# Performance work log

Measured on AMD Instinct MI355X. Metric: run time of the kernel, lower is better.

The kernel has to match this reference:

```python
import jax, jax.numpy as jnp
import numpy as np

B, E, V, L = 16384, 16, 1_000_000, 50
DENSE, ONEHOT, MULTIHOT = 13, 26, 2
UNITS = [64, 12]
NN_IN = E * (ONEHOT + MULTIHOT) + DENSE  # 16*28+13 = 461
CONCAT_IN = 1 + E + UNITS[-1]            # 29


def setup_inputs() -> dict:
    key = jax.random.key(0)
    ks = jax.random.split(key, 12)
    s = 0.02  # glorot-ish init scale
    return {
        "dense": jax.random.normal(ks[0], (B, DENSE), jnp.float32),
        "onehot": jax.random.randint(ks[1], (B, ONEHOT), 0, V, jnp.int32),
        "multihot_ids": jax.random.randint(ks[2], (B, MULTIHOT, L), 0, V, jnp.int32),
        "multihot_mask": jnp.ones((B, MULTIHOT, L), jnp.float32),
        "fm_w": jax.random.normal(ks[3], (V, 1), jnp.float32) * s,
        "fm_emb": jax.random.normal(ks[4], (V, E), jnp.float32) * s,
        "nn_w0": jax.random.normal(ks[5], (NN_IN, UNITS[0]), jnp.float32) * s,
        "nn_b0": jnp.zeros((UNITS[0],), jnp.float32),
        "nn_w1": jax.random.normal(ks[6], (UNITS[0], UNITS[1]), jnp.float32) * s,
        "nn_b1": jnp.zeros((UNITS[1],), jnp.float32),
        "concat_w": jax.random.normal(ks[7], (CONCAT_IN, 1), jnp.float32) * s,
        "concat_b": jnp.zeros((1,), jnp.float32),
    }


def reference(dense, onehot, multihot_ids, multihot_mask, fm_w, fm_emb,
              nn_w0, nn_b0, nn_w1, nn_b1, concat_w, concat_b):
    # --- embedding lookups ---
    onehot_emb = fm_emb[onehot]                      # [B, 26, E]
    mh_emb = fm_emb[multihot_ids]                    # [B, 2, L, E]
    m = multihot_mask[..., None]                     # [B, 2, L, 1]
    # embedding_lookup_sparse(combiner='mean') over valid slots; empty rows -> 0 (tf.pad)
    denom = jnp.maximum(jnp.sum(m, axis=2), 1.0)     # [B, 2, 1]
    multihot_emb = jnp.sum(mh_emb * m, axis=2) / denom  # [B, 2, E]
    cat_emb = jnp.concatenate([onehot_emb, multihot_emb], axis=1)  # [B, 28, E]

    # --- FM 1st order: sum_i w_i (x_i = 1) ---
    fm_1st = jnp.sum(fm_w[onehot], axis=1)           # [B, 1]

    # --- FM 2nd order (keep_k_dims=True): 0.5*((sum v)^2 - sum v^2) ---
    s = jnp.sum(cat_emb, axis=1)                     # [B, E]
    fm_2nd = 0.5 * (s * s - jnp.sum(cat_emb * cat_emb, axis=1))  # [B, E]

    # --- deep part ---
    nn_inp = jnp.concatenate([cat_emb.reshape(-1, E * (ONEHOT + MULTIHOT)), dense], axis=1)
    h = jax.nn.relu(nn_inp @ nn_w0 + nn_b0)
    h = jax.nn.relu(h @ nn_w1 + nn_b1)               # [B, 12]

    concat_inp = jnp.concatenate([fm_1st, fm_2nd, h], axis=1)  # [B, 29]
    return jax.nn.sigmoid(concat_inp @ concat_w + concat_b)    # [B, 1]
```

## Files before the change

### kernel.cpp

```cpp
#include <hip/hip_runtime.h>
#include <hip/hip_bf16.h>

#define BATCH 16384
#define EDIM  16
#define NOH   26
#define LL    50
#define KIN   461
#define KPAD  480
#define KLDS  488

using bf16x8 = __attribute__((ext_vector_type(8))) short;
using f32x4  = __attribute__((ext_vector_type(4))) float;

static __device__ __forceinline__ unsigned short f2bf(float f) {
    union { float f; unsigned int u; } v; v.f = f;
    unsigned int r = v.u + 0x7FFFu + ((v.u >> 16) & 1u);
    return (unsigned short)(r >> 16);
}

__global__ __launch_bounds__(1024) void fused(
    const float* __restrict__ dense,
    const int*   __restrict__ onehot,
    const int*   __restrict__ mh_ids,
    const float* __restrict__ mh_mask,
    const float* __restrict__ fm_w,
    const float* __restrict__ fm_emb,
    const float* __restrict__ w0,
    const float* __restrict__ b0,
    const float* __restrict__ w1,
    const float* __restrict__ b1,
    const float* __restrict__ concat_w,
    const float* __restrict__ concat_b,
    float* __restrict__ out)
{
    __shared__ unsigned short As[64 * KLDS];
    __shared__ unsigned short w0s[30720];
    __shared__ float h0s[64][68];
    __shared__ float w1t[12 * 64];
    __shared__ float part_s[64];
    __shared__ float b0s[64];
    __shared__ float b1s[12];
    __shared__ float cwh[12];

    const int t  = threadIdx.x;
    const int wv = t >> 6;
    const int l  = t & 63;
    const int s  = l >> 2;
    const int d  = l & 3;
    const int row0 = blockIdx.x << 6;

    for (int idx = t; idx < 30720; idx += 1024) {
        int j    = idx & 7;
        int frag = idx >> 3;
        int lane = frag & 63;
        int tile = frag >> 6;
        int nt = tile / 15;
        int kt = tile - nt * 15;
        int k = kt * 32 + ((lane >> 4) << 3) + j;
        int n = (nt << 4) + (lane & 15);
        float v = (k < KIN) ? w0[k * 64 + n] : 0.f;
        w0s[idx] = f2bf(v);
    }
    if (t < 768) { int k = t / 12, j = t - k * 12; w1t[j * 64 + k] = w1[t]; }
    if (t < 64)  b0s[t] = b0[t];
    if (t >= 64 && t < 76)   b1s[t - 64] = b1[t - 64];
    if (t >= 96 && t < 108)  cwh[t - 96] = concat_w[17 + (t - 96)];

    for (int i = 0; i < 4; ++i) {
        const int r = (wv << 2) + i;
        const int b = row0 + r;

        const float v1 = (s < 10) ? 1.f : 0.f;
        int oid0 = onehot[b * NOH + s];
        int oid1 = (s < 10) ? onehot[b * NOH + 16 + s] : 0;

        int   mid[7]; float mmk[7];
        #pragma unroll
        for (int p = 0; p < 7; ++p) {
            int pi = p * 16 + s;
            bool valid = pi < 100;
            int f = (pi >= 50) ? 1 : 0;
            int ii = pi - f * 50;
            size_t off = ((size_t)b * 2 + f) * LL + ii;
            mid[p] = valid ? mh_ids[off]  : 0;
            mmk[p] = valid ? mh_mask[off] : 0.f;
        }

        float4 e0 = *(const float4*)(fm_emb + (size_t)oid0 * EDIM + d * 4);
        float4 e1 = *(const float4*)(fm_emb + (size_t)oid1 * EDIM + d * 4);
        float  wsa = fm_w[oid0];
        float  wsb = fm_w[oid1];
        float4 gm[7];
        #pragma unroll
        for (int p = 0; p < 7; ++p)
            gm[p] = *(const float4*)(fm_emb + (size_t)mid[p] * EDIM + d * 4);

        e1.x *= v1; e1.y *= v1; e1.z *= v1; e1.w *= v1;
        float wsum = (d == 0) ? (wsa + v1 * wsb) : 0.f;

        unsigned short* rowp = As + r * KLDS;
        {
            ushort4 u; u.x = f2bf(e0.x); u.y = f2bf(e0.y); u.z = f2bf(e0.z); u.w = f2bf(e0.w);
            *(ushort4*)(rowp + s * EDIM + d * 4) = u;
        }
        if (s < 10) {
            ushort4 u; u.x = f2bf(e1.x); u.y = f2bf(e1.y); u.z = f2bf(e1.z); u.w = f2bf(e1.w);
            *(ushort4*)(rowp + (16 + s) * EDIM + d * 4) = u;
        }

        float a0x=0,a0y=0,a0z=0,a0w=0, a1x=0,a1y=0,a1z=0,a1w=0, m0=0, m1=0;
        #pragma unroll
        for (int p = 0; p < 7; ++p) {
            int pi = p * 16 + s;
            float m = mmk[p];
            if (pi >= 50) { a1x += m*gm[p].x; a1y += m*gm[p].y; a1z += m*gm[p].z; a1w += m*gm[p].w; m1 += m; }
            else          { a0x += m*gm[p].x; a0y += m*gm[p].y; a0z += m*gm[p].z; a0w += m*gm[p].w; m0 += m; }
        }

        float ohx = e0.x + e1.x, ohy = e0.y + e1.y, ohz = e0.z + e1.z, ohw = e0.w + e1.w;
        float qx = e0.x*e0.x + e1.x*e1.x, qy = e0.y*e0.y + e1.y*e1.y;
        float qz = e0.z*e0.z + e1.z*e1.z, qw = e0.w*e0.w + e1.w*e1.w;

#define R4(v) { v += __shfl_xor(v, 4); v += __shfl_xor(v, 8); v += __shfl_xor(v, 16); v += __shfl_xor(v, 32); }
        R4(a0x) R4(a0y) R4(a0z) R4(a0w)
        R4(a1x) R4(a1y) R4(a1z) R4(a1w)
        R4(m0)  R4(m1)
        R4(ohx) R4(ohy) R4(ohz) R4(ohw)
        R4(qx)  R4(qy)  R4(qz)  R4(qw)
        R4(wsum)
#undef R4

        float inv0 = 1.f / fmaxf(m0, 1.f);
        float inv1 = 1.f / fmaxf(m1, 1.f);
        float h0x = a0x*inv0, h0y = a0y*inv0, h0z = a0z*inv0, h0w = a0w*inv0;
        float h1x = a1x*inv1, h1y = a1y*inv1, h1z = a1z*inv1, h1w = a1w*inv1;

        if (s == 0) {
            ushort4 u; u.x = f2bf(h0x); u.y = f2bf(h0y); u.z = f2bf(h0z); u.w = f2bf(h0w);
            *(ushort4*)(rowp + 26 * EDIM + d * 4) = u;
        }
        if (s == 1) {
            ushort4 u; u.x = f2bf(h1x); u.y = f2bf(h1y); u.z = f2bf(h1z); u.w = f2bf(h1w);
            *(ushort4*)(rowp + 27 * EDIM + d * 4) = u;
        }

        float sx = ohx + h0x + h1x, sy = ohy + h0y + h1y, sz = ohz + h0z + h1z, sw = ohw + h0w + h1w;
        float tx = qx + h0x*h0x + h1x*h1x, ty = qy + h0y*h0y + h1y*h1y;
        float tz = qz + h0z*h0z + h1z*h1z, tw = qw + h0w*h0w + h1w*h1w;
        float f2x = 0.5f * (sx*sx - tx), f2y = 0.5f * (sy*sy - ty);
        float f2z = 0.5f * (sz*sz - tz), f2w = 0.5f * (sw*sw - tw);

        float cw0 = concat_w[0];
        float c0 = concat_w[1 + d*4 + 0], c1 = concat_w[1 + d*4 + 1];
        float c2 = concat_w[1 + d*4 + 2], c3 = concat_w[1 + d*4 + 3];
        float part = f2x*c0 + f2y*c1 + f2z*c2 + f2w*c3 + wsum * cw0;
        part += __shfl_xor(part, 1);
        part += __shfl_xor(part, 2);
        if (l == 0) part_s[r] = part + concat_b[0];

        if (l < 32) {
            float v = (l < 13) ? dense[b * 13 + l] : 0.f;
            rowp[448 + l] = f2bf(v);
        }
    }
    __syncthreads();

    const int rt = wv >> 2, nt = wv & 3;
    const int c = l & 15, g = l >> 4;

    f32x4 acc = {0.f, 0.f, 0.f, 0.f};
    const unsigned short* ap = As + (rt * 16 + c) * KLDS + (g << 3);
    const bf16x8* bp = (const bf16x8*)w0s + nt * 15 * 64 + l;

    #pragma unroll
    for (int kt = 0; kt < 15; ++kt) {
        bf16x8 a = *(const bf16x8*)(ap + kt * 32);
        acc = __builtin_amdgcn_mfma_f32_16x16x32_bf16(a, bp[kt * 64], acc, 0, 0, 0);
    }

    #pragma unroll
    for (int reg = 0; reg < 4; ++reg)
        h0s[rt * 16 + g * 4 + reg][nt * 16 + c] = fmaxf(acc[reg] + b0s[nt * 16 + c], 0.f);
    __syncthreads();

    if (wv < 4) {
        float s0 = b1s[g*3 + 0], s1 = b1s[g*3 + 1], s2 = b1s[g*3 + 2];
        #pragma unroll
        for (int k4 = 0; k4 < 16; ++k4) {
            float4 h  = *(const float4*)&h0s[wv * 16 + c][k4 * 4];
            float4 wa = *(const float4*)&w1t[(g*3 + 0) * 64 + k4 * 4];
            float4 wb = *(const float4*)&w1t[(g*3 + 1) * 64 + k4 * 4];
            float4 wc = *(const float4*)&w1t[(g*3 + 2) * 64 + k4 * 4];
            s0 += h.x*wa.x + h.y*wa.y + h.z*wa.z + h.w*wa.w;
            s1 += h.x*wb.x + h.y*wb.y + h.z*wb.z + h.w*wb.w;
            s2 += h.x*wc.x + h.y*wc.y + h.z*wc.z + h.w*wc.w;
        }
        float hd = fmaxf(s0, 0.f)*cwh[g*3] + fmaxf(s1, 0.f)*cwh[g*3+1] + fmaxf(s2, 0.f)*cwh[g*3+2];
        hd += __shfl_xor(hd, 16);
        hd += __shfl_xor(hd, 32);
        if (g == 0) {
            int rr = row0 + wv * 16 + c;
            float x = part_s[wv * 16 + c] + hd;
            out[rr] = 1.f / (1.f + __expf(-x));
        }
    }
}

extern "C" void kernel_launch(void* const* d_in, const int* in_sizes, int n_in,
                              void* d_out, int out_size, void* d_ws, size_t ws_size,
                              hipStream_t stream) {
    const float* dense   = (const float*)d_in[0];
    const int*   onehot  = (const int*)  d_in[1];
    const int*   mh_ids  = (const int*)  d_in[2];
    const float* mh_mask = (const float*)d_in[3];
    const float* fm_w    = (const float*)d_in[4];
    const float* fm_emb  = (const float*)d_in[5];
    const float* w0      = (const float*)d_in[6];
    const float* b0      = (const float*)d_in[7];
    const float* w1      = (const float*)d_in[8];
    const float* b1      = (const float*)d_in[9];
    const float* cw      = (const float*)d_in[10];
    const float* cb      = (const float*)d_in[11];

    hipLaunchKernelGGL(fused, dim3(BATCH / 64), dim3(1024), 0, stream,
                       dense, onehot, mh_ids, mh_mask, fm_w, fm_emb,
                       w0, b0, w1, b1, cw, cb, (float*)d_out);
}
```

Baseline: 165.0 us.

## Pre-swizzle W0 to bf16 in a prep kernel and shrink blocks to 32 rows

A small prep kernel converts and swizzles W0 into MFMA fragment order in workspace once per call, so each block no longer rebuilds a 60KB LDS copy. The fused kernel now handles 32 rows per block with 512 threads, reads W0 fragments straight from global memory (L2-resident), and stores the hidden layer as bf16. The goal is to cut per-block LDS footprint and setup work so more blocks can stay resident and the gather latency is hidden better. In exchange it adds an extra launch, more global or L2 traffic for W0, and some extra rounding of the hidden activations.

```diff
diff --git a/kernel.cpp b/kernel.cpp
--- a/kernel.cpp
+++ b/kernel.cpp
@@ -8,6 +8,7 @@
 #define KIN   461
 #define KPAD  480
 #define KLDS  488
+#define ROWS  32
 
 using bf16x8 = __attribute__((ext_vector_type(8))) short;
 using f32x4  = __attribute__((ext_vector_type(4))) float;
@@ -17,39 +18,15 @@
     unsigned int r = v.u + 0x7FFFu + ((v.u >> 16) & 1u);
     return (unsigned short)(r >> 16);
 }
-
-__global__ __launch_bounds__(1024) void fused(
-    const float* __restrict__ dense,
-    const int*   __restrict__ onehot,
-    const int*   __restrict__ mh_ids,
-    const float* __restrict__ mh_mask,
-    const float* __restrict__ fm_w,
-    const float* __restrict__ fm_emb,
-    const float* __restrict__ w0,
-    const float* __restrict__ b0,
-    const float* __restrict__ w1,
-    const float* __restrict__ b1,
-    const float* __restrict__ concat_w,
-    const float* __restrict__ concat_b,
-    float* __restrict__ out)
-{
-    __shared__ unsigned short As[64 * KLDS];
-    __shared__ unsigned short w0s[30720];
-    __shared__ float h0s[64][68];
-    __shared__ float w1t[12 * 64];
-    __shared__ float part_s[64];
-    __shared__ float b0s[64];
-    __shared__ float b1s[12];
-    __shared__ float cwh[12];
-
-    const int t  = threadIdx.x;
-    const int wv = t >> 6;
-    const int l  = t & 63;
-    const int s  = l >> 2;
-    const int d  = l & 3;
-    const int row0 = blockIdx.x << 6;
-
-    for (int idx = t; idx < 30720; idx += 1024) {
+static __device__ __forceinline__ float bf2f(unsigned short u) {
+    union { unsigned int u; float f; } v; v.u = ((unsigned int)u) << 16;
+    return v.f;
+}
+
+__global__ __launch_bounds__(256) void prep(const float* __restrict__ w0,
+                                            unsigned short* __restrict__ w0f) {
+    int idx = blockIdx.x * 256 + threadIdx.x;
+    if (idx < 30720) {
         int j    = idx & 7;
         int frag = idx >> 3;
         int lane = frag & 63;
@@ -59,12 +36,44 @@
         int k = kt * 32 + ((lane >> 4) << 3) + j;
         int n = (nt << 4) + (lane & 15);
         float v = (k < KIN) ? w0[k * 64 + n] : 0.f;
-        w0s[idx] = f2bf(v);
-    }
-    if (t < 768) { int k = t / 12, j = t - k * 12; w1t[j * 64 + k] = w1[t]; }
-    if (t < 64)  b0s[t] = b0[t];
-    if (t >= 64 && t < 76)   b1s[t - 64] = b1[t - 64];
-    if (t >= 96 && t < 108)  cwh[t - 96] = concat_w[17 + (t - 96)];
+        w0f[idx] = f2bf(v);
+    }
+}
+
+__global__ __launch_bounds__(512, 4) void fused(
+    const float* __restrict__ dense,
+    const int*   __restrict__ onehot,
+    const int*   __restrict__ mh_ids,
+    const float* __restrict__ mh_mask,
+    const float* __restrict__ fm_w,
+    const float* __restrict__ fm_emb,
+    const unsigned short* __restrict__ w0f,
+    const float* __restrict__ b0,
+    const float* __restrict__ w1,
+    const float* __restrict__ b1,
+    const float* __restrict__ concat_w,
+    const float* __restrict__ concat_b,
+    float* __restrict__ out)
+{
+    __shared__ unsigned short As[ROWS * KLDS];
+    __shared__ unsigned short h0s[ROWS][68];
+    __shared__ float w1t[12 * 64];
+    __shared__ float part_s[ROWS];
+    __shared__ float b0s[64];
+    __shared__ float b1s[12];
+    __shared__ float cwh[12];
+
+    const int t  = threadIdx.x;
+    const int wv = t >> 6;
+    const int l  = t & 63;
+    const int s  = l >> 2;
+    const int d  = l & 3;
+    const int row0 = blockIdx.x << 5;
+
+    for (int i = t; i < 768; i += 512) { int k = i / 12, j = i - k * 12; w1t[j * 64 + k] = w1[i]; }
+    if (t < 64)               b0s[t] = b0[t];
+    if (t >= 64 && t < 76)    b1s[t - 64] = b1[t - 64];
+    if (t >= 96 && t < 108)   cwh[t - 96] = concat_w[17 + (t - 96)];
 
     for (int i = 0; i < 4; ++i) {
         const int r = (wv << 2) + i;
@@ -170,30 +179,36 @@
 
     f32x4 acc = {0.f, 0.f, 0.f, 0.f};
     const unsigned short* ap = As + (rt * 16 + c) * KLDS + (g << 3);
-    const bf16x8* bp = (const bf16x8*)w0s + nt * 15 * 64 + l;
+    const unsigned short* bgp = w0f + ((size_t)(nt * 15) * 64 + l) * 8;
 
     #pragma unroll
     for (int kt = 0; kt < 15; ++kt) {
         bf16x8 a = *(const bf16x8*)(ap + kt * 32);
-        acc = __builtin_amdgcn_mfma_f32_16x16x32_bf16(a, bp[kt * 64], acc, 0, 0, 0);
+        bf16x8 bb = *(const bf16x8*)(bgp + (size_t)kt * 64 * 8);
+        acc = __builtin_amdgcn_mfma_f32_16x16x32_bf16(a, bb, acc, 0, 0, 0);
     }
 
     #pragma unroll
     for (int reg = 0; reg < 4; ++reg)
-        h0s[rt * 16 + g * 4 + reg][nt * 16 + c] = fmaxf(acc[reg] + b0s[nt * 16 + c], 0.f);
+        h0s[rt * 16 + g * 4 + reg][nt * 16 + c] = f2bf(fmaxf(acc[reg] + b0s[nt * 16 + c], 0.f));
     __syncthreads();
 
-    if (wv < 4) {
+    if (wv < 2) {
         float s0 = b1s[g*3 + 0], s1 = b1s[g*3 + 1], s2 = b1s[g*3 + 2];
-        #pragma unroll
-        for (int k4 = 0; k4 < 16; ++k4) {
-            float4 h  = *(const float4*)&h0s[wv * 16 + c][k4 * 4];
-            float4 wa = *(const float4*)&w1t[(g*3 + 0) * 64 + k4 * 4];
-            float4 wb = *(const float4*)&w1t[(g*3 + 1) * 64 + k4 * 4];
-            float4 wc = *(const float4*)&w1t[(g*3 + 2) * 64 + k4 * 4];
-            s0 += h.x*wa.x + h.y*wa.y + h.z*wa.z + h.w*wa.w;
-            s1 += h.x*wb.x + h.y*wb.y + h.z*wb.z + h.w*wb.w;
-            s2 += h.x*wc.x + h.y*wc.y + h.z*wc.z + h.w*wc.w;
+        const unsigned short* hrow = &h0s[wv * 16 + c][0];
+        #pragma unroll
+        for (int k8 = 0; k8 < 8; ++k8) {
+            ushort4 ha = *(const ushort4*)(hrow + k8 * 8 + 0);
+            ushort4 hb = *(const ushort4*)(hrow + k8 * 8 + 4);
+            float h[8] = { bf2f(ha.x), bf2f(ha.y), bf2f(ha.z), bf2f(ha.w),
+                           bf2f(hb.x), bf2f(hb.y), bf2f(hb.z), bf2f(hb.w) };
+            #pragma unroll
+            for (int j = 0; j < 8; ++j) {
+                int k = k8 * 8 + j;
+                s0 += h[j] * w1t[(g*3 + 0) * 64 + k];
+                s1 += h[j] * w1t[(g*3 + 1) * 64 + k];
+                s2 += h[j] * w1t[(g*3 + 2) * 64 + k];
+            }
         }
         float hd = fmaxf(s0, 0.f)*cwh[g*3] + fmaxf(s1, 0.f)*cwh[g*3+1] + fmaxf(s2, 0.f)*cwh[g*3+2];
         hd += __shfl_xor(hd, 16);
@@ -222,7 +237,10 @@
     const float* cw      = (const float*)d_in[10];
     const float* cb      = (const float*)d_in[11];
 
-    hipLaunchKernelGGL(fused, dim3(BATCH / 64), dim3(1024), 0, stream,
+    unsigned short* w0f = (unsigned short*)d_ws;
+
+    hipLaunchKernelGGL(prep, dim3(120), dim3(256), 0, stream, w0, w0f);
+    hipLaunchKernelGGL(fused, dim3(BATCH / ROWS), dim3(512), 0, stream,
                        dense, onehot, mh_ids, mh_mask, fm_w, fm_emb,
-                       w0, b0, w1, b1, cw, cb, (float*)d_out);
-}
+                       w0f, b0, w1, b1, cw, cb, (float*)d_out);
+}
```

Result: faster. 159.1 us (-3.5%).
